# Kernel tuning notes

Measured on AMD Instinct MI355X. Metric: run time of the kernel, lower is better.

Reference implementation:

```python
import math
import jax, jax.numpy as jnp
import numpy as np

D = 256      # embedding_dim (= internal_dim, downsample_rate 1)
H = 8        # num_heads
HD = D // H  # head_dim = 32
NTC = 16     # num_text_classes
NIMG = 4096  # image tokens (64x64)
N = NIMG + NTC
B = 2
NKE = 64     # num_k_exclude_rope


def _rope(x, freqs):
    # x: (b, h, n, c); freqs: (n, c//2, 2) = (cos, sin) of complex rotary factors
    b, h, n, c = x.shape
    xp = x.reshape(b, h, n, c // 2, 2)
    cos, sin = freqs[..., 0], freqs[..., 1]
    xr, xi = xp[..., 0], xp[..., 1]
    out_r = xr * cos - xi * sin
    out_i = xr * sin + xi * cos
    return jnp.stack([out_r, out_i], axis=-1).reshape(b, h, n, c)


def _sep_heads(x):
    b, n, c = x.shape
    return x.reshape(b, n, H, c // H).transpose(0, 2, 1, 3)  # (b,h,n,hd)


def setup_inputs() -> dict:
    key = jax.random.key(0)
    ks = jax.random.split(key, 14)
    s = 0.02
    # rotary factors: unit-norm cos/sin pairs
    ang_img = jax.random.uniform(ks[3], (NIMG, HD // 2)) * (2.0 * np.pi)
    ang_txt = jax.random.uniform(ks[4], (NTC, HD // 2)) * (2.0 * np.pi)
    return {
        "q": jax.random.normal(ks[0], (B, N, D), dtype=jnp.float32),
        "k": jax.random.normal(ks[1], (B, N, D), dtype=jnp.float32),
        "v": jax.random.normal(ks[2], (B, N, D), dtype=jnp.float32),
        "freqs_cis_img": jnp.stack([jnp.cos(ang_img), jnp.sin(ang_img)], axis=-1),
        "freqs_cis_txt": jnp.stack([jnp.cos(ang_txt), jnp.sin(ang_txt)], axis=-1),
        "Wq": jax.random.normal(ks[5], (D, D), dtype=jnp.float32) * s,
        "bq": jnp.zeros((D,), dtype=jnp.float32),
        "Wk": jax.random.normal(ks[6], (D, D), dtype=jnp.float32) * s,
        "bk": jnp.zeros((D,), dtype=jnp.float32),
        "Wv": jax.random.normal(ks[7], (D, D), dtype=jnp.float32) * s,
        "bv": jnp.zeros((D,), dtype=jnp.float32),
        "Wo": jax.random.normal(ks[8], (D, D), dtype=jnp.float32) * s,
        "bo": jnp.zeros((D,), dtype=jnp.float32),
        "num_k_exclude_rope": NKE,
    }


def reference(q, k, v, freqs_cis_img, freqs_cis_txt,
              Wq, bq, Wk, bk, Wv, bv, Wo, bo, num_k_exclude_rope):
    q = q @ Wq.T + bq
    k = k @ Wk.T + bk
    v = v @ Wv.T + bv
    q = _sep_heads(q)  # (b,h,n,hd)
    k = _sep_heads(k)
    v = _sep_heads(v)

    # split tokens into image / text regions, apply RoPE separately
    q_img, q_txt = q[:, :, :-NTC, :], q[:, :, -NTC:, :]
    k_img, k_txt = k[:, :, :-NTC, :], k[:, :, -NTC:, :]
    q_img = _rope(q_img, freqs_cis_img)
    k_img = _rope(k_img, freqs_cis_img)
    q_txt = _rope(q_txt, freqs_cis_txt)
    k_txt = _rope(k_txt, freqs_cis_txt)
    q = jnp.concatenate([q_img, q_txt], axis=-2)
    k = jnp.concatenate([k_img, k_txt], axis=-2)

    scale = 1.0 / math.sqrt(HD)
    nke = num_k_exclude_rope
    if nke > 0:
        k_td, k_mem = k[:, :, :-nke, :], k[:, :, -nke:, :]
        v_td, v_mem = v[:, :, :-nke, :], v[:, :, -nke:, :]
        attn = jax.nn.softmax(jnp.einsum('bhqd,bhkd->bhqk', q, k_td) * scale, axis=-1)
        out = jnp.einsum('bhqk,bhkd->bhqd', attn, v_td)
        attn_m = jax.nn.softmax(jnp.einsum('bhqd,bhkd->bhqk', q, k_mem) * scale, axis=-1)
        out = out + jnp.einsum('bhqk,bhkd->bhqd', attn_m, v_mem)
    else:
        attn = jax.nn.softmax(jnp.einsum('bhqd,bhkd->bhqk', q, k) * scale, axis=-1)
        out = jnp.einsum('bhqk,bhkd->bhqd', attn, v)

    b, h, n, hd = out.shape
    out = out.transpose(0, 2, 1, 3).reshape(b, n, h * hd)
    return out @ Wo.T + bo
```

## Files before the change

kernel.cpp:

```cpp
#include <hip/hip_runtime.h>
#include <hip/hip_bf16.h>

#define BN    4112
#define NKR   4160
#define BB    2
#define HH    8
#define NIMG_ 4096
#define NMAIN 4048
#define MROWS 8224
#define VPH   4160
#define QSCALE 0.25505402f

typedef __attribute__((ext_vector_type(8))) short short8;
typedef __attribute__((ext_vector_type(4))) float f32x4;

__device__ __forceinline__ unsigned short f2bs(float x) { return __bfloat16_as_ushort(__float2bfloat16(x)); }
__device__ __forceinline__ unsigned pkbf(float a, float b) {
    __hip_bfloat162 h = __float22bfloat162_rn(make_float2(a, b));
    unsigned u; __builtin_memcpy(&u, &h, 4); return u;
}
__device__ __forceinline__ float fexp2(float x) {
#if __has_builtin(__builtin_amdgcn_exp2f)
    return __builtin_amdgcn_exp2f(x);
#else
    return exp2f(x);
#endif
}
__device__ __forceinline__ f32x4 mfma16(short8 a, short8 b, f32x4 c) {
    return __builtin_amdgcn_mfma_f32_16x16x32_bf16(a, b, c, 0, 0, 0);
}

__global__ __launch_bounds__(256)
void qkv_mfma(const float* __restrict__ Aq, const float* __restrict__ Ak, const float* __restrict__ Av,
              const float* __restrict__ Wq, const float* __restrict__ Wk, const float* __restrict__ Wv,
              const float* __restrict__ bq, const float* __restrict__ bk, const float* __restrict__ bv,
              short* __restrict__ Qr, short* __restrict__ Kr, short* __restrict__ Vt,
              const float* __restrict__ fimg, const float* __restrict__ ftxt)
{
    __shared__ __align__(16) short Ws[2][64][72];
    __shared__ __align__(16) short Ds[2][64][72];

    const int mode = blockIdx.z;
    const float* A    = (mode == 0) ? Aq : (mode == 1) ? Ak : Av;
    const float* W    = (mode == 0) ? Wq : (mode == 1) ? Wk : Wv;
    const float* bias = (mode == 0) ? bq : (mode == 1) ? bk : bv;

    const int t    = threadIdx.x;
    const int wave = t >> 6, lane = t & 63, q16 = lane & 15, quad = lane >> 4;
    const int f0 = blockIdx.x * 64;
    const int m0 = blockIdx.y * 64;
    const int sr = t >> 2, sc = (t & 3) * 16;
    const int arow = m0 + sr;
    const bool aval = arow < MROWS;
    const float* wp = W + (size_t)(f0 + sr) * 256 + sc;
    const float* ap = A + (size_t)(aval ? arow : 0) * 256 + sc;

    f32x4 acc[4] = {{0,0,0,0},{0,0,0,0},{0,0,0,0},{0,0,0,0}};

    uint4 wr0, wr1, dr0, dr1;
    {
        float4 a0 = *(const float4*)(wp),     a1 = *(const float4*)(wp + 4);
        float4 a2 = *(const float4*)(wp + 8), a3 = *(const float4*)(wp + 12);
        wr0 = uint4{pkbf(a0.x,a0.y), pkbf(a0.z,a0.w), pkbf(a1.x,a1.y), pkbf(a1.z,a1.w)};
        wr1 = uint4{pkbf(a2.x,a2.y), pkbf(a2.z,a2.w), pkbf(a3.x,a3.y), pkbf(a3.z,a3.w)};
        a0 = *(const float4*)(ap);     a1 = *(const float4*)(ap + 4);
        a2 = *(const float4*)(ap + 8); a3 = *(const float4*)(ap + 12);
        dr0 = uint4{pkbf(a0.x,a0.y), pkbf(a0.z,a0.w), pkbf(a1.x,a1.y), pkbf(a1.z,a1.w)};
        dr1 = uint4{pkbf(a2.x,a2.y), pkbf(a2.z,a2.w), pkbf(a3.x,a3.y), pkbf(a3.z,a3.w)};
    }
    *(uint4*)&Ws[0][sr][sc] = wr0; *(uint4*)&Ws[0][sr][sc + 8] = wr1;
    *(uint4*)&Ds[0][sr][sc] = dr0; *(uint4*)&Ds[0][sr][sc + 8] = dr1;
    __syncthreads();

    #pragma unroll
    for (int ki = 0; ki < 4; ++ki) {
        const int buf = ki & 1;
        if (ki < 3) {
            const int k1 = (ki + 1) * 64;
            float4 a0 = *(const float4*)(wp + k1),     a1 = *(const float4*)(wp + k1 + 4);
            float4 a2 = *(const float4*)(wp + k1 + 8), a3 = *(const float4*)(wp + k1 + 12);
            wr0 = uint4{pkbf(a0.x,a0.y), pkbf(a0.z,a0.w), pkbf(a1.x,a1.y), pkbf(a1.z,a1.w)};
            wr1 = uint4{pkbf(a2.x,a2.y), pkbf(a2.z,a2.w), pkbf(a3.x,a3.y), pkbf(a3.z,a3.w)};
            a0 = *(const float4*)(ap + k1);     a1 = *(const float4*)(ap + k1 + 4);
            a2 = *(const float4*)(ap + k1 + 8); a3 = *(const float4*)(ap + k1 + 12);
            dr0 = uint4{pkbf(a0.x,a0.y), pkbf(a0.z,a0.w), pkbf(a1.x,a1.y), pkbf(a1.z,a1.w)};
            dr1 = uint4{pkbf(a2.x,a2.y), pkbf(a2.z,a2.w), pkbf(a3.x,a3.y), pkbf(a3.z,a3.w)};
        }
        #pragma unroll
        for (int ks = 0; ks < 2; ++ks) {
            const short8 af = *(const short8*)&Ws[buf][wave * 16 + q16][ks * 32 + quad * 8];
            #pragma unroll
            for (int ct = 0; ct < 4; ++ct) {
                const short8 bf = *(const short8*)&Ds[buf][ct * 16 + q16][ks * 32 + quad * 8];
                acc[ct] = mfma16(af, bf, acc[ct]);
            }
        }
        if (ki < 3) {
            *(uint4*)&Ws[buf ^ 1][sr][sc] = wr0; *(uint4*)&Ws[buf ^ 1][sr][sc + 8] = wr1;
            *(uint4*)&Ds[buf ^ 1][sr][sc] = dr0; *(uint4*)&Ds[buf ^ 1][sr][sc + 8] = dr1;
            __syncthreads();
        }
    }

    const int fbase = f0 + wave * 16 + quad * 4;
    const float4 bb = *(const float4*)(bias + fbase);
    float vs[4][4];
    #pragma unroll
    for (int ct = 0; ct < 4; ++ct) {
        int n = m0 + ct * 16 + q16;
        float v0 = acc[ct][0] + bb.x, v1 = acc[ct][1] + bb.y;
        float v2 = acc[ct][2] + bb.z, v3 = acc[ct][3] + bb.w;
        int b  = (n >= BN) ? 1 : 0;
        int nb = n - b * BN;
        if (mode < 2) {
            int j0 = (fbase & 31) >> 1;
            const float* fr = (nb < NIMG_) ? (fimg + ((size_t)nb * 16 + j0) * 2)
                                           : (ftxt + ((size_t)(nb - NIMG_) * 16 + j0) * 2);
            float4 cs = *(const float4*)fr;
            float r0 = v0 * cs.x - v1 * cs.y, i0 = v0 * cs.y + v1 * cs.x;
            float r1 = v2 * cs.z - v3 * cs.w, i1 = v2 * cs.w + v3 * cs.z;
            v0 = r0; v1 = i0; v2 = r1; v3 = i1;
        }
        if (mode == 2) {
            vs[ct][0] = v0; vs[ct][1] = v1; vs[ct][2] = v2; vs[ct][3] = v3;
            continue;
        }
        if (n >= MROWS) continue;
        const int h = (fbase >> 5) & 7, hd = fbase & 31;
        if (mode == 0) {
            unsigned short* op = (unsigned short*)Qr + (((size_t)(b * HH + h) * BN + nb) * 32 + hd);
            *(uint2*)op = uint2{pkbf(v0 * QSCALE, v1 * QSCALE), pkbf(v2 * QSCALE, v3 * QSCALE)};
        } else {
            int nk = nb + ((nb >= NMAIN) ? 48 : 0);
            unsigned short* op = (unsigned short*)Kr + (((size_t)(b * HH + h) * NKR + nk) * 32 + hd);
            *(uint2*)op = uint2{pkbf(v0, v1), pkbf(v2, v3)};
        }
    }

    if (mode == 2) {
        short (*Tr)[72] = Ds[0];
        const int fl = wave * 16 + quad * 4;
        #pragma unroll
        for (int ct = 0; ct < 4; ++ct) {
            const int nl = ct * 16 + q16;
            Tr[fl + 0][nl] = (short)f2bs(vs[ct][0]);
            Tr[fl + 1][nl] = (short)f2bs(vs[ct][1]);
            Tr[fl + 2][nl] = (short)f2bs(vs[ct][2]);
            Tr[fl + 3][nl] = (short)f2bs(vs[ct][3]);
        }
        __syncthreads();
        const int h0 = (f0 >> 5) & 7;
        #pragma unroll
        for (int ii = 0; ii < 2; ++ii) {
            const int r  = ii * 32 + (t >> 3);
            const int c8 = (t & 7) * 8;
            const int ng = m0 + c8;
            if (ng < MROWS) {
                int b  = (ng >= BN) ? 1 : 0;
                int nb = ng - b * BN;
                int h  = h0 + (r >> 5), hd = r & 31;
                size_t hdbase = ((size_t)(b * HH + h) * 32 + hd) * VPH;
                #pragma unroll
                for (int j = 0; j < 2; ++j) {
                    int nb4 = nb + j * 4;
                    int nk  = nb4 + ((nb4 >= NMAIN) ? 48 : 0);
                    int c = nk >> 5, within = nk & 31;
                    int slot = ((within >> 2) & 3) * 8 + ((within >> 4) & 1) * 4;
                    uint2 val = *(const uint2*)&Tr[r][c8 + j * 4];
                    *(uint2*)((unsigned short*)Vt + hdbase + c * 32 + slot) = val;
                }
            }
        }
    }

    if (blockIdx.x == 0 && blockIdx.y < 16) {
        const int bh = blockIdx.y;
        if (mode == 1 && t < 192) {
            short* base = Kr + (size_t)bh * NKR * 32 + (size_t)NMAIN * 32;
            *(uint4*)(base + t * 8) = uint4{0u, 0u, 0u, 0u};
        } else if (mode == 2) {
            for (int i = t; i < 384; i += 256) {
                int hd = i / 12, u = i % 12;
                size_t base = ((size_t)bh * 32 + hd) * VPH;
                int c, slot;
                if (u < 4) { c = 126; slot = 4 + u * 8; }
                else       { c = 127; slot = (u - 4) * 4; }
                *(uint2*)((unsigned short*)Vt + base + c * 32 + slot) = uint2{0u, 0u};
            }
        }
    }
}

__global__ __launch_bounds__(128, 4)
void attn_mfma(const short* __restrict__ Qr, const short* __restrict__ Kr,
               const short* __restrict__ Vp, unsigned short* __restrict__ AO)
{
    __shared__ float ex[64][20];

    const int t = threadIdx.x;
    const int wave = t >> 6, lane = t & 63, q16 = lane & 15, quad = lane >> 4;
    const int bh = blockIdx.y;
    const int qb = blockIdx.x * 32;
    const int q0 = qb + q16, q1 = qb + 16 + q16;
    const int q0c = (q0 < BN) ? q0 : BN - 1;
    const int q1c = (q1 < BN) ? q1 : BN - 1;
    const short8 qf0 = *(const short8*)(Qr + ((size_t)bh * BN + q0c) * 32 + quad * 8);
    const short8 qf1 = *(const short8*)(Qr + ((size_t)bh * BN + q1c) * 32 + quad * 8);

    const short* kp  = Kr + (size_t)bh * NKR * 32 + (size_t)wave * 65 * 1024 + q16 * 32 + quad * 8;
    const short* vb  = Vp + (size_t)bh * 32 * VPH + (size_t)wave * 65 * 32 + quad * 8;
    const short* vp0 = vb + (size_t)q16 * VPH;
    const short* vp1 = vb + (size_t)(16 + q16) * VPH;

    f32x4 o00 = {0,0,0,0}, o01 = {0,0,0,0}, o10 = {0,0,0,0}, o11 = {0,0,0,0};
    f32x4 m00 = {0,0,0,0}, m01 = {0,0,0,0}, m10 = {0,0,0,0}, m11 = {0,0,0,0};
    float LA0 = 0.f, LA1 = 0.f, LB0 = 0.f, LB1 = 0.f;

    const int ng = 65 - wave * 2;

    short8 kc0 = *(const short8*)(kp);
    short8 kc1 = *(const short8*)(kp + 512);
    short8 vc0 = *(const short8*)(vp0);
    short8 vc1 = *(const short8*)(vp1);

    for (int g = 0; g < ng; ++g) {
        short8 kn0 = kc0, kn1 = kc1, vn0 = vc0, vn1 = vc1;
        if (g + 1 < ng) {
            kn0 = *(const short8*)(kp + (g + 1) * 1024);
            kn1 = *(const short8*)(kp + (g + 1) * 1024 + 512);
            vn0 = *(const short8*)(vp0 + (g + 1) * 32);
            vn1 = *(const short8*)(vp1 + (g + 1) * 32);
        }
        const f32x4 z = {0,0,0,0};
        f32x4 s00 = mfma16(kc0, qf0, z), s01 = mfma16(kc0, qf1, z);
        f32x4 s10 = mfma16(kc1, qf0, z), s11 = mfma16(kc1, qf1, z);
        float a0 = fexp2(s00[0]), a1 = fexp2(s00[1]), a2 = fexp2(s00[2]), a3 = fexp2(s00[3]);
        float b0 = fexp2(s10[0]), b1 = fexp2(s10[1]), b2 = fexp2(s10[2]), b3 = fexp2(s10[3]);
        float c0 = fexp2(s01[0]), c1 = fexp2(s01[1]), c2 = fexp2(s01[2]), c3 = fexp2(s01[3]);
        float d0 = fexp2(s11[0]), d1 = fexp2(s11[1]), d2 = fexp2(s11[2]), d3 = fexp2(s11[3]);
        LA0 += ((a0 + a1) + (a2 + a3)) + ((b0 + b1) + (b2 + b3));
        LA1 += ((c0 + c1) + (c2 + c3)) + ((d0 + d1) + (d2 + d3));
        uint4 p0u = uint4{pkbf(a0, a1), pkbf(a2, a3), pkbf(b0, b1), pkbf(b2, b3)};
        uint4 p1u = uint4{pkbf(c0, c1), pkbf(c2, c3), pkbf(d0, d1), pkbf(d2, d3)};
        short8 pb0, pb1;
        __builtin_memcpy(&pb0, &p0u, 16); __builtin_memcpy(&pb1, &p1u, 16);
        o00 = mfma16(vc0, pb0, o00); o01 = mfma16(vc0, pb1, o01);
        o10 = mfma16(vc1, pb0, o10); o11 = mfma16(vc1, pb1, o11);
        kc0 = kn0; kc1 = kn1; vc0 = vn0; vc1 = vn1;
    }

    if (wave == 1) {
        const short* kpm  = Kr + (size_t)bh * NKR * 32 + (size_t)4096 * 32 + q16 * 32 + quad * 8;
        const short* vbm  = Vp + (size_t)bh * 32 * VPH + 128 * 32 + quad * 8;
        const short* vm0  = vbm + (size_t)q16 * VPH;
        const short* vm1  = vbm + (size_t)(16 + q16) * VPH;
        #pragma unroll
        for (int g = 0; g < 2; ++g) {
            short8 k0 = *(const short8*)(kpm + g * 1024);
            short8 k1 = *(const short8*)(kpm + g * 1024 + 512);
            short8 v0 = *(const short8*)(vm0 + g * 32);
            short8 v1 = *(const short8*)(vm1 + g * 32);
            const f32x4 z = {0,0,0,0};
            f32x4 s00 = mfma16(k0, qf0, z), s01 = mfma16(k0, qf1, z);
            f32x4 s10 = mfma16(k1, qf0, z), s11 = mfma16(k1, qf1, z);
            float a0 = fexp2(s00[0]), a1 = fexp2(s00[1]), a2 = fexp2(s00[2]), a3 = fexp2(s00[3]);
            float b0 = fexp2(s10[0]), b1 = fexp2(s10[1]), b2 = fexp2(s10[2]), b3 = fexp2(s10[3]);
            float c0 = fexp2(s01[0]), c1 = fexp2(s01[1]), c2 = fexp2(s01[2]), c3 = fexp2(s01[3]);
            float d0 = fexp2(s11[0]), d1 = fexp2(s11[1]), d2 = fexp2(s11[2]), d3 = fexp2(s11[3]);
            LB0 += ((a0 + a1) + (a2 + a3)) + ((b0 + b1) + (b2 + b3));
            LB1 += ((c0 + c1) + (c2 + c3)) + ((d0 + d1) + (d2 + d3));
            uint4 p0u = uint4{pkbf(a0, a1), pkbf(a2, a3), pkbf(b0, b1), pkbf(b2, b3)};
            uint4 p1u = uint4{pkbf(c0, c1), pkbf(c2, c3), pkbf(d0, d1), pkbf(d2, d3)};
            short8 pb0, pb1;
            __builtin_memcpy(&pb0, &p0u, 16); __builtin_memcpy(&pb1, &p1u, 16);
            m00 = mfma16(v0, pb0, m00); m01 = mfma16(v0, pb1, m01);
            m10 = mfma16(v1, pb0, m10); m11 = mfma16(v1, pb1, m11);
        }
    }

    LA0 += __shfl_xor(LA0, 16); LA0 += __shfl_xor(LA0, 32);
    LA1 += __shfl_xor(LA1, 16); LA1 += __shfl_xor(LA1, 32);
    LB0 += __shfl_xor(LB0, 16); LB0 += __shfl_xor(LB0, 32);
    LB1 += __shfl_xor(LB1, 16); LB1 += __shfl_xor(LB1, 32);

    if (wave == 0) {
        *(f32x4*)&ex[lane][0]  = o00;
        *(f32x4*)&ex[lane][4]  = o10;
        *(f32x4*)&ex[lane][8]  = o01;
        *(f32x4*)&ex[lane][12] = o11;
        ex[lane][16] = LA0; ex[lane][17] = LA1;
    }
    __syncthreads();

    if (wave == 1) {
        const int b = bh >> 3, h = bh & 7;
        const float iA0 = 1.f / (LA0 + ex[lane][16] - 48.f);
        const float iA1 = 1.f / (LA1 + ex[lane][17] - 48.f);
        const float iB0 = 1.f / LB0, iB1 = 1.f / LB1;
        if (q0 < BN) {
            unsigned short* ap = AO + ((size_t)b * BN + q0) * 256 + h * 32;
            float w0[4], w1[4];
            #pragma unroll
            for (int r = 0; r < 4; ++r) {
                w0[r] = (o00[r] + ex[lane][r])     * iA0 + m00[r] * iB0;
                w1[r] = (o10[r] + ex[lane][4 + r]) * iA0 + m10[r] * iB0;
            }
            *(uint2*)(ap + quad * 4)      = uint2{pkbf(w0[0], w0[1]), pkbf(w0[2], w0[3])};
            *(uint2*)(ap + 16 + quad * 4) = uint2{pkbf(w1[0], w1[1]), pkbf(w1[2], w1[3])};
        }
        if (q1 < BN) {
            unsigned short* ap = AO + ((size_t)b * BN + q1) * 256 + h * 32;
            float w0[4], w1[4];
            #pragma unroll
            for (int r = 0; r < 4; ++r) {
                w0[r] = (o01[r] + ex[lane][8 + r])  * iA1 + m01[r] * iB1;
                w1[r] = (o11[r] + ex[lane][12 + r]) * iA1 + m11[r] * iB1;
            }
            *(uint2*)(ap + quad * 4)      = uint2{pkbf(w0[0], w0[1]), pkbf(w0[2], w0[3])};
            *(uint2*)(ap + 16 + quad * 4) = uint2{pkbf(w1[0], w1[1]), pkbf(w1[2], w1[3])};
        }
    }
}

__global__ __launch_bounds__(256)
void gemm_out(const unsigned short* __restrict__ A, const float* __restrict__ W,
              const float* __restrict__ bias, float* __restrict__ out)
{
    __shared__ __align__(16) short Ws[2][64][72];
    __shared__ __align__(16) short Ds[2][64][72];
    const int t    = threadIdx.x;
    const int wave = t >> 6, lane = t & 63, q16 = lane & 15, quad = lane >> 4;
    const int f0 = blockIdx.x * 64, m0 = blockIdx.y * 64;
    const int sr = t >> 2, sc = (t & 3) * 16;
    const int arow = m0 + sr;
    const bool aval = arow < MROWS;
    const float* wp = W + (size_t)(f0 + sr) * 256 + sc;
    const unsigned short* ap = A + (size_t)(aval ? arow : 0) * 256 + sc;

    f32x4 acc[4] = {{0,0,0,0},{0,0,0,0},{0,0,0,0},{0,0,0,0}};

    uint4 wr0, wr1, dr0, dr1;
    {
        float4 a0 = *(const float4*)(wp),     a1 = *(const float4*)(wp + 4);
        float4 a2 = *(const float4*)(wp + 8), a3 = *(const float4*)(wp + 12);
        wr0 = uint4{pkbf(a0.x,a0.y), pkbf(a0.z,a0.w), pkbf(a1.x,a1.y), pkbf(a1.z,a1.w)};
        wr1 = uint4{pkbf(a2.x,a2.y), pkbf(a2.z,a2.w), pkbf(a3.x,a3.y), pkbf(a3.z,a3.w)};
        dr0 = *(const uint4*)(ap); dr1 = *(const uint4*)(ap + 8);
    }
    *(uint4*)&Ws[0][sr][sc] = wr0; *(uint4*)&Ws[0][sr][sc + 8] = wr1;
    *(uint4*)&Ds[0][sr][sc] = dr0; *(uint4*)&Ds[0][sr][sc + 8] = dr1;
    __syncthreads();

    #pragma unroll
    for (int ki = 0; ki < 4; ++ki) {
        const int buf = ki & 1;
        if (ki < 3) {
            const int k1 = (ki + 1) * 64;
            float4 a0 = *(const float4*)(wp + k1),     a1 = *(const float4*)(wp + k1 + 4);
            float4 a2 = *(const float4*)(wp + k1 + 8), a3 = *(const float4*)(wp + k1 + 12);
            wr0 = uint4{pkbf(a0.x,a0.y), pkbf(a0.z,a0.w), pkbf(a1.x,a1.y), pkbf(a1.z,a1.w)};
            wr1 = uint4{pkbf(a2.x,a2.y), pkbf(a2.z,a2.w), pkbf(a3.x,a3.y), pkbf(a3.z,a3.w)};
            dr0 = *(const uint4*)(ap + k1); dr1 = *(const uint4*)(ap + k1 + 8);
        }
        #pragma unroll
        for (int ks = 0; ks < 2; ++ks) {
            const short8 af = *(const short8*)&Ws[buf][wave * 16 + q16][ks * 32 + quad * 8];
            #pragma unroll
            for (int ct = 0; ct < 4; ++ct) {
                const short8 bf = *(const short8*)&Ds[buf][ct * 16 + q16][ks * 32 + quad * 8];
                acc[ct] = mfma16(af, bf, acc[ct]);
            }
        }
        if (ki < 3) {
            *(uint4*)&Ws[buf ^ 1][sr][sc] = wr0; *(uint4*)&Ws[buf ^ 1][sr][sc + 8] = wr1;
            *(uint4*)&Ds[buf ^ 1][sr][sc] = dr0; *(uint4*)&Ds[buf ^ 1][sr][sc + 8] = dr1;
            __syncthreads();
        }
    }

    const int fbase = f0 + wave * 16 + quad * 4;
    const float4 bb = *(const float4*)(bias + fbase);
    #pragma unroll
    for (int ct = 0; ct < 4; ++ct) {
        int n = m0 + ct * 16 + q16;
        if (n >= MROWS) continue;
        float* op = out + (size_t)n * 256 + fbase;
        *(float4*)op = float4{acc[ct][0] + bb.x, acc[ct][1] + bb.y,
                              acc[ct][2] + bb.z, acc[ct][3] + bb.w};
    }
}

extern "C" void kernel_launch(void* const* d_in, const int* in_sizes, int n_in,
                              void* d_out, int out_size, void* d_ws, size_t ws_size,
                              hipStream_t stream)
{
    (void)in_sizes; (void)n_in; (void)out_size; (void)ws_size;
    const float* q    = (const float*)d_in[0];
    const float* k    = (const float*)d_in[1];
    const float* v    = (const float*)d_in[2];
    const float* fimg = (const float*)d_in[3];
    const float* ftxt = (const float*)d_in[4];
    const float* Wq   = (const float*)d_in[5];
    const float* bq   = (const float*)d_in[6];
    const float* Wk   = (const float*)d_in[7];
    const float* bk   = (const float*)d_in[8];
    const float* Wv   = (const float*)d_in[9];
    const float* bv   = (const float*)d_in[10];
    const float* Wo   = (const float*)d_in[11];
    const float* bo   = (const float*)d_in[12];

    char* w = (char*)d_ws;
    short*          Qr = (short*)(w);
    short*          Kr = (short*)(w + 4210688);
    short*          Vp = (short*)(w + 8470528);
    unsigned short* AO = (unsigned short*)(w + 12730368);

    qkv_mfma<<<dim3(4, 129, 3), 256, 0, stream>>>(q, k, v, Wq, Wk, Wv, bq, bk, bv,
                                                  Qr, Kr, Vp, fimg, ftxt);
    attn_mfma<<<dim3(129, 16), 128, 0, stream>>>(Qr, Kr, Vp, AO);
    gemm_out<<<dim3(4, 129), 256, 0, stream>>>(AO, Wo, bo, (float*)d_out);
}
```

Baseline: 224.8 us.

## Split attention key range across four waves with LDS reduction

The attention kernel now runs 256 threads per block, so four waves each handle 32 key groups instead of two waves handling about 65. The memory-key tail moves to wave 3, which normalizes it up front. Partial outputs and row sums are combined through shared memory by wave 0. The main loop is unrolled two-deep with double-buffered loads and interleaved per-query-tile compute. The aim is shorter serial chains per wave and better latency hiding, at the cost of more LDS traffic and a larger reduction step.

```diff
diff --git a/kernel.cpp b/kernel.cpp
--- a/kernel.cpp
+++ b/kernel.cpp
@@ -191,11 +191,13 @@
     }
 }
 
-__global__ __launch_bounds__(128, 4)
+__global__ __launch_bounds__(256, 5)
 void attn_mfma(const short* __restrict__ Qr, const short* __restrict__ Kr,
                const short* __restrict__ Vp, unsigned short* __restrict__ AO)
 {
-    __shared__ float ex[64][20];
+    __shared__ float exO[4][32][36];
+    __shared__ float exM[32][36];
+    __shared__ float exL[4][32];
 
     const int t = threadIdx.x;
     const int wave = t >> 6, lane = t & 63, q16 = lane & 15, quad = lane >> 4;
@@ -207,53 +209,13 @@
     const short8 qf0 = *(const short8*)(Qr + ((size_t)bh * BN + q0c) * 32 + quad * 8);
     const short8 qf1 = *(const short8*)(Qr + ((size_t)bh * BN + q1c) * 32 + quad * 8);
 
-    const short* kp  = Kr + (size_t)bh * NKR * 32 + (size_t)wave * 65 * 1024 + q16 * 32 + quad * 8;
-    const short* vb  = Vp + (size_t)bh * 32 * VPH + (size_t)wave * 65 * 32 + quad * 8;
-    const short* vp0 = vb + (size_t)q16 * VPH;
-    const short* vp1 = vb + (size_t)(16 + q16) * VPH;
-
-    f32x4 o00 = {0,0,0,0}, o01 = {0,0,0,0}, o10 = {0,0,0,0}, o11 = {0,0,0,0};
-    f32x4 m00 = {0,0,0,0}, m01 = {0,0,0,0}, m10 = {0,0,0,0}, m11 = {0,0,0,0};
-    float LA0 = 0.f, LA1 = 0.f, LB0 = 0.f, LB1 = 0.f;
-
-    const int ng = 65 - wave * 2;
-
-    short8 kc0 = *(const short8*)(kp);
-    short8 kc1 = *(const short8*)(kp + 512);
-    short8 vc0 = *(const short8*)(vp0);
-    short8 vc1 = *(const short8*)(vp1);
-
-    for (int g = 0; g < ng; ++g) {
-        short8 kn0 = kc0, kn1 = kc1, vn0 = vc0, vn1 = vc1;
-        if (g + 1 < ng) {
-            kn0 = *(const short8*)(kp + (g + 1) * 1024);
-            kn1 = *(const short8*)(kp + (g + 1) * 1024 + 512);
-            vn0 = *(const short8*)(vp0 + (g + 1) * 32);
-            vn1 = *(const short8*)(vp1 + (g + 1) * 32);
-        }
-        const f32x4 z = {0,0,0,0};
-        f32x4 s00 = mfma16(kc0, qf0, z), s01 = mfma16(kc0, qf1, z);
-        f32x4 s10 = mfma16(kc1, qf0, z), s11 = mfma16(kc1, qf1, z);
-        float a0 = fexp2(s00[0]), a1 = fexp2(s00[1]), a2 = fexp2(s00[2]), a3 = fexp2(s00[3]);
-        float b0 = fexp2(s10[0]), b1 = fexp2(s10[1]), b2 = fexp2(s10[2]), b3 = fexp2(s10[3]);
-        float c0 = fexp2(s01[0]), c1 = fexp2(s01[1]), c2 = fexp2(s01[2]), c3 = fexp2(s01[3]);
-        float d0 = fexp2(s11[0]), d1 = fexp2(s11[1]), d2 = fexp2(s11[2]), d3 = fexp2(s11[3]);
-        LA0 += ((a0 + a1) + (a2 + a3)) + ((b0 + b1) + (b2 + b3));
-        LA1 += ((c0 + c1) + (c2 + c3)) + ((d0 + d1) + (d2 + d3));
-        uint4 p0u = uint4{pkbf(a0, a1), pkbf(a2, a3), pkbf(b0, b1), pkbf(b2, b3)};
-        uint4 p1u = uint4{pkbf(c0, c1), pkbf(c2, c3), pkbf(d0, d1), pkbf(d2, d3)};
-        short8 pb0, pb1;
-        __builtin_memcpy(&pb0, &p0u, 16); __builtin_memcpy(&pb1, &p1u, 16);
-        o00 = mfma16(vc0, pb0, o00); o01 = mfma16(vc0, pb1, o01);
-        o10 = mfma16(vc1, pb0, o10); o11 = mfma16(vc1, pb1, o11);
-        kc0 = kn0; kc1 = kn1; vc0 = vn0; vc1 = vn1;
-    }
-
-    if (wave == 1) {
-        const short* kpm  = Kr + (size_t)bh * NKR * 32 + (size_t)4096 * 32 + q16 * 32 + quad * 8;
-        const short* vbm  = Vp + (size_t)bh * 32 * VPH + 128 * 32 + quad * 8;
-        const short* vm0  = vbm + (size_t)q16 * VPH;
-        const short* vm1  = vbm + (size_t)(16 + q16) * VPH;
+    if (wave == 3) {
+        const short* kpm = Kr + (size_t)bh * NKR * 32 + (size_t)4096 * 32 + q16 * 32 + quad * 8;
+        const short* vbm = Vp + (size_t)bh * 32 * VPH + 128 * 32 + quad * 8;
+        const short* vm0 = vbm + (size_t)q16 * VPH;
+        const short* vm1 = vbm + (size_t)(16 + q16) * VPH;
+        f32x4 m00 = {0,0,0,0}, m01 = {0,0,0,0}, m10 = {0,0,0,0}, m11 = {0,0,0,0};
+        float LB0 = 0.f, LB1 = 0.f;
         #pragma unroll
         for (int g = 0; g < 2; ++g) {
             short8 k0 = *(const short8*)(kpm + g * 1024);
@@ -276,34 +238,96 @@
             m00 = mfma16(v0, pb0, m00); m01 = mfma16(v0, pb1, m01);
             m10 = mfma16(v1, pb0, m10); m11 = mfma16(v1, pb1, m11);
         }
+        LB0 += __shfl_xor(LB0, 16); LB0 += __shfl_xor(LB0, 32);
+        LB1 += __shfl_xor(LB1, 16); LB1 += __shfl_xor(LB1, 32);
+        const float iB0 = 1.f / LB0, iB1 = 1.f / LB1;
+        #pragma unroll
+        for (int r = 0; r < 4; ++r) {
+            exM[q16][quad * 4 + r]           = m00[r] * iB0;
+            exM[q16][16 + quad * 4 + r]      = m10[r] * iB0;
+            exM[16 + q16][quad * 4 + r]      = m01[r] * iB1;
+            exM[16 + q16][16 + quad * 4 + r] = m11[r] * iB1;
+        }
+    }
+
+    const short* kp  = Kr + (size_t)bh * NKR * 32 + (size_t)wave * 32 * 1024 + q16 * 32 + quad * 8;
+    const short* vb  = Vp + (size_t)bh * 32 * VPH + (size_t)wave * 32 * 32 + quad * 8;
+    const short* vp0 = vb + (size_t)q16 * VPH;
+    const short* vp1 = vb + (size_t)(16 + q16) * VPH;
+
+    f32x4 o00 = {0,0,0,0}, o01 = {0,0,0,0}, o10 = {0,0,0,0}, o11 = {0,0,0,0};
+    float LA0 = 0.f, LA1 = 0.f;
+
+    auto loadc = [&](int g, short8& k0, short8& k1, short8& v0, short8& v1) {
+        k0 = *(const short8*)(kp + (size_t)g * 1024);
+        k1 = *(const short8*)(kp + (size_t)g * 1024 + 512);
+        v0 = *(const short8*)(vp0 + g * 32);
+        v1 = *(const short8*)(vp1 + g * 32);
+    };
+    auto compute = [&](short8 k0, short8 k1, short8 v0, short8 v1) {
+        const f32x4 z = {0,0,0,0};
+        f32x4 s00 = mfma16(k0, qf0, z), s10 = mfma16(k1, qf0, z);
+        float a0 = fexp2(s00[0]), a1 = fexp2(s00[1]), a2 = fexp2(s00[2]), a3 = fexp2(s00[3]);
+        float b0 = fexp2(s10[0]), b1 = fexp2(s10[1]), b2 = fexp2(s10[2]), b3 = fexp2(s10[3]);
+        LA0 += ((a0 + a1) + (a2 + a3)) + ((b0 + b1) + (b2 + b3));
+        uint4 p0u = uint4{pkbf(a0, a1), pkbf(a2, a3), pkbf(b0, b1), pkbf(b2, b3)};
+        short8 pb0; __builtin_memcpy(&pb0, &p0u, 16);
+        o00 = mfma16(v0, pb0, o00); o10 = mfma16(v1, pb0, o10);
+        f32x4 s01 = mfma16(k0, qf1, z), s11 = mfma16(k1, qf1, z);
+        float c0 = fexp2(s01[0]), c1 = fexp2(s01[1]), c2 = fexp2(s01[2]), c3 = fexp2(s01[3]);
+        float d0 = fexp2(s11[0]), d1 = fexp2(s11[1]), d2 = fexp2(s11[2]), d3 = fexp2(s11[3]);
+        LA1 += ((c0 + c1) + (c2 + c3)) + ((d0 + d1) + (d2 + d3));
+        uint4 p1u = uint4{pkbf(c0, c1), pkbf(c2, c3), pkbf(d0, d1), pkbf(d2, d3)};
+        short8 pb1; __builtin_memcpy(&pb1, &p1u, 16);
+        o01 = mfma16(v0, pb1, o01); o11 = mfma16(v1, pb1, o11);
+    };
+
+    short8 ka0, ka1, va0, va1, kb0, kb1, vb0, vb1;
+    loadc(0, ka0, ka1, va0, va1);
+    loadc(1, kb0, kb1, vb0, vb1);
+    #pragma unroll 1
+    for (int g = 0; g < 32; g += 2) {
+        compute(ka0, ka1, va0, va1);
+        if (g + 2 < 32) loadc(g + 2, ka0, ka1, va0, va1);
+        compute(kb0, kb1, vb0, vb1);
+        if (g + 3 < 32) loadc(g + 3, kb0, kb1, vb0, vb1);
     }
 
     LA0 += __shfl_xor(LA0, 16); LA0 += __shfl_xor(LA0, 32);
     LA1 += __shfl_xor(LA1, 16); LA1 += __shfl_xor(LA1, 32);
-    LB0 += __shfl_xor(LB0, 16); LB0 += __shfl_xor(LB0, 32);
-    LB1 += __shfl_xor(LB1, 16); LB1 += __shfl_xor(LB1, 32);
+
+    if (wave != 0) {
+        #pragma unroll
+        for (int r = 0; r < 4; ++r) {
+            exO[wave][q16][quad * 4 + r]           = o00[r];
+            exO[wave][q16][16 + quad * 4 + r]      = o10[r];
+            exO[wave][16 + q16][quad * 4 + r]      = o01[r];
+            exO[wave][16 + q16][16 + quad * 4 + r] = o11[r];
+        }
+        if (quad == 0) { exL[wave][q16] = LA0; exL[wave][16 + q16] = LA1; }
+    }
+    __syncthreads();
 
     if (wave == 0) {
-        *(f32x4*)&ex[lane][0]  = o00;
-        *(f32x4*)&ex[lane][4]  = o10;
-        *(f32x4*)&ex[lane][8]  = o01;
-        *(f32x4*)&ex[lane][12] = o11;
-        ex[lane][16] = LA0; ex[lane][17] = LA1;
-    }
-    __syncthreads();
-
-    if (wave == 1) {
+        float LA0t = LA0 - 48.f, LA1t = LA1 - 48.f;
+        #pragma unroll
+        for (int w2 = 1; w2 < 4; ++w2) {
+            o00 += *(const f32x4*)&exO[w2][q16][quad * 4];
+            o10 += *(const f32x4*)&exO[w2][q16][16 + quad * 4];
+            o01 += *(const f32x4*)&exO[w2][16 + q16][quad * 4];
+            o11 += *(const f32x4*)&exO[w2][16 + q16][16 + quad * 4];
+            LA0t += exL[w2][q16];
+            LA1t += exL[w2][16 + q16];
+        }
+        const float iA0 = 1.f / LA0t, iA1 = 1.f / LA1t;
         const int b = bh >> 3, h = bh & 7;
-        const float iA0 = 1.f / (LA0 + ex[lane][16] - 48.f);
-        const float iA1 = 1.f / (LA1 + ex[lane][17] - 48.f);
-        const float iB0 = 1.f / LB0, iB1 = 1.f / LB1;
         if (q0 < BN) {
             unsigned short* ap = AO + ((size_t)b * BN + q0) * 256 + h * 32;
             float w0[4], w1[4];
             #pragma unroll
             for (int r = 0; r < 4; ++r) {
-                w0[r] = (o00[r] + ex[lane][r])     * iA0 + m00[r] * iB0;
-                w1[r] = (o10[r] + ex[lane][4 + r]) * iA0 + m10[r] * iB0;
+                w0[r] = o00[r] * iA0 + exM[q16][quad * 4 + r];
+                w1[r] = o10[r] * iA0 + exM[q16][16 + quad * 4 + r];
             }
             *(uint2*)(ap + quad * 4)      = uint2{pkbf(w0[0], w0[1]), pkbf(w0[2], w0[3])};
             *(uint2*)(ap + 16 + quad * 4) = uint2{pkbf(w1[0], w1[1]), pkbf(w1[2], w1[3])};
@@ -313,8 +337,8 @@
             float w0[4], w1[4];
             #pragma unroll
             for (int r = 0; r < 4; ++r) {
-                w0[r] = (o01[r] + ex[lane][8 + r])  * iA1 + m01[r] * iB1;
-                w1[r] = (o11[r] + ex[lane][12 + r]) * iA1 + m11[r] * iB1;
+                w0[r] = o01[r] * iA1 + exM[16 + q16][quad * 4 + r];
+                w1[r] = o11[r] * iA1 + exM[16 + q16][16 + quad * 4 + r];
             }
             *(uint2*)(ap + quad * 4)      = uint2{pkbf(w0[0], w0[1]), pkbf(w0[2], w0[3])};
             *(uint2*)(ap + 16 + quad * 4) = uint2{pkbf(w1[0], w1[1]), pkbf(w1[2], w1[3])};
@@ -417,6 +441,6 @@
 
     qkv_mfma<<<dim3(4, 129, 3), 256, 0, stream>>>(q, k, v, Wq, Wk, Wv, bq, bk, bv,
                                                   Qr, Kr, Vp, fimg, ftxt);
-    attn_mfma<<<dim3(129, 16), 128, 0, stream>>>(Qr, Kr, Vp, AO);
+    attn_mfma<<<dim3(129, 16), 256, 0, stream>>>(Qr, Kr, Vp, AO);
     gemm_out<<<dim3(4, 129), 256, 0, stream>>>(AO, Wo, bo, (float*)d_out);
 }
```

New measurement: 335.3 us. 49.2% more time.
